# Optimization experiments

Hardware: AMD Instinct MI355X
Metric: run time of the kernel (lower is better)

The kernel has to match this reference:

```python
import jax, jax.numpy as jnp
import numpy as np

B, N, D_MODEL, H = 8, 1024, 768, 12
HD = D_MODEL // H  # head dim = 64
SCALE = D_MODEL ** (-0.5)  # NOTE: original scales by input_dim**-0.5, not head_dim**-0.5


def setup_inputs() -> dict:
    key = jax.random.key(0)
    k1, k2 = jax.random.split(key)
    x = jax.random.normal(k1, (B, N, D_MODEL), dtype=jnp.float32)
    # torch Linear weight is [out,in]; we store transposed [in,out] for x @ W
    w_qkv = jax.random.normal(k2, (D_MODEL, 3 * D_MODEL), dtype=jnp.float32) * (D_MODEL ** -0.5)
    b_qkv = jnp.zeros((3 * D_MODEL,), dtype=jnp.float32)
    return {"x": x, "w_qkv": w_qkv, "b_qkv": b_qkv}


def reference(x, w_qkv, b_qkv):
    # QKV projection: [B, N, 3*D]
    y = jnp.einsum("bnd,de->bne", x, w_qkv) + b_qkv
    # Faithful to einops 'b n (h d qkv) -> qkv b h n d': qkv is fastest-varying
    y = y.reshape(B, N, H, HD, 3)
    q = jnp.transpose(y[..., 0], (0, 2, 1, 3))  # [B, H, N, HD]
    k = jnp.transpose(y[..., 1], (0, 2, 1, 3))
    v = jnp.transpose(y[..., 2], (0, 2, 1, 3))
    energy = jnp.einsum("bhqd,bhkd->bhqk", q, k)
    attn = jax.nn.softmax(energy * SCALE, axis=-1)  # dropout is identity at eval
    out = jnp.einsum("bhqk,bhkd->bhqd", attn, v)
    # 'b h n d -> b n (h d)'
    return jnp.transpose(out, (0, 2, 1, 3)).reshape(B, N, D_MODEL)
```

## Files before the change

kernel.cpp:

```cpp
#include <hip/hip_runtime.h>
#include <hip/hip_bf16.h>
#include <stdint.h>

#define NB 8
#define NS 1024
#define DM 768
#define NH 12
#define DH 64
#define NE 2304
#define MTOT (NB*NS)

typedef unsigned short u16;
typedef __attribute__((ext_vector_type(8))) __bf16 bf16x8;
typedef __attribute__((ext_vector_type(4))) float floatx4;

#define WS_XB  0ull
#define WS_WT  12582912ull
#define WS_QB  16121856ull
#define WS_KB  28704768ull
#define WS_VT  41287680ull

__device__ __forceinline__ u16 f2bf(float f) {
  union { float f; uint32_t u; } v; v.f = f;
  uint32_t r = (v.u + 0x7fffu + ((v.u >> 16) & 1u)) >> 16;
  return (u16)r;
}

__device__ __forceinline__ void gload16(const void* g, void* l) {
  __builtin_amdgcn_global_load_lds(
      (const __attribute__((address_space(1))) void*)g,
      (__attribute__((address_space(3))) void*)l, 16, 0, 0);
}

__global__ void conv_x_kernel(const float4* __restrict__ x, u16* __restrict__ xb, int n4) {
  int i = blockIdx.x * blockDim.x + threadIdx.x;
  int stride = gridDim.x * blockDim.x;
  for (; i < n4; i += stride) {
    float4 v = x[i];
    ushort4 r;
    r.x = f2bf(v.x); r.y = f2bf(v.y); r.z = f2bf(v.z); r.w = f2bf(v.w);
    ((ushort4*)xb)[i] = r;
  }
}

__global__ void transpose_w_kernel(const float* __restrict__ w, u16* __restrict__ wt) {
  __shared__ float tile[32][33];
  const int e0 = blockIdx.x * 32, k0 = blockIdx.y * 32;
  const int tx = threadIdx.x, ty = threadIdx.y;
#pragma unroll
  for (int i = 0; i < 4; i++)
    tile[ty + i*8][tx] = w[(size_t)(k0 + ty + i*8) * NE + e0 + tx];
  __syncthreads();
#pragma unroll
  for (int i = 0; i < 4; i++)
    wt[(size_t)(e0 + ty + i*8) * DM + k0 + tx] = f2bf(tile[tx][ty + i*8]);
}

__global__ __launch_bounds__(256) void qkv_gemm_kernel(
    const u16* __restrict__ xb, const u16* __restrict__ wt,
    const float* __restrict__ bias,
    u16* __restrict__ qb, u16* __restrict__ kb, u16* __restrict__ vtb) {
  __shared__ __align__(16) u16 a_lds[128 * 32];
  __shared__ __align__(16) u16 b_lds[128 * 32];
  const int t  = threadIdx.x;
  const int w  = t >> 6, l = t & 63;
  const int wr = w >> 1, wc = w & 1;
  const int lq = l & 15, lg = l >> 4;
  const int m0 = (int)(blockIdx.x % 64) * 128;
  const int n0 = (int)(blockIdx.x / 64) * 128;

  floatx4 z = {0.f, 0.f, 0.f, 0.f};
  floatx4 acc[4][4];
#pragma unroll
  for (int i = 0; i < 4; i++)
#pragma unroll
    for (int j = 0; j < 4; j++) acc[i][j] = z;

  const int srow = t >> 2;
  const int scb  = (t & 3) ^ ((t >> 3) & 3);
  const u16* ga = xb + (size_t)m0 * DM + scb * 8;
  const u16* gb = wt + (size_t)n0 * DM + scb * 8;
  const int rswz = (lq >> 1) & 3;

  for (int k0 = 0; k0 < DM; k0 += 32) {
#pragma unroll
    for (int i = 0; i < 2; i++) {
      gload16(ga + (size_t)(i*64 + srow) * DM + k0, (char*)a_lds + i*4096 + w*1024);
      gload16(gb + (size_t)(i*64 + srow) * DM + k0, (char*)b_lds + i*4096 + w*1024);
    }
    __syncthreads();

    bf16x8 af[4], bfr[4];
#pragma unroll
    for (int i = 0; i < 4; i++)
      af[i] = *(const bf16x8*)((const char*)a_lds + (wr*64 + i*16 + lq)*64 + ((lg ^ rswz) * 16));
#pragma unroll
    for (int j = 0; j < 4; j++)
      bfr[j] = *(const bf16x8*)((const char*)b_lds + (wc*64 + j*16 + lq)*64 + ((lg ^ rswz) * 16));
#pragma unroll
    for (int i = 0; i < 4; i++)
#pragma unroll
      for (int j = 0; j < 4; j++)
        acc[i][j] = __builtin_amdgcn_mfma_f32_16x16x32_bf16(af[i], bfr[j], acc[i][j], 0, 0, 0);
    __syncthreads();
  }

#pragma unroll
  for (int j = 0; j < 4; j++) {
    const int gn = n0 + wc*64 + j*16 + lq;
    const float bv = bias[gn];
    const int qkv = gn % 3;
    const int h   = gn / 192;
    const int d   = (gn % 192) / 3;
#pragma unroll
    for (int i = 0; i < 4; i++) {
      const int gmb = m0 + wr*64 + i*16 + lg*4;
#pragma unroll
      for (int r = 0; r < 4; r++) {
        const int gm = gmb + r;
        const int bb = gm >> 10, nn = gm & 1023;
        const int bh = bb * NH + h;
        const u16 val = f2bf(acc[i][j][r] + bv);
        if (qkv == 0)      qb[((size_t)bh * NS + nn) * DH + d] = val;
        else if (qkv == 1) kb[((size_t)bh * NS + nn) * DH + d] = val;
        else               vtb[((size_t)bh * DH + d) * NS + nn] = val;
      }
    }
  }
}

__global__ __launch_bounds__(256) void attn_kernel(
    const u16* __restrict__ qb, const u16* __restrict__ kb,
    const u16* __restrict__ vtb, float* __restrict__ out) {
  __shared__ __align__(16) u16 k_lds[64 * 64];
  __shared__ __align__(16) u16 v_lds[64 * 64];
  __shared__ __align__(16) u16 p_lds[4][16 * 40];

  const int t = threadIdx.x, w = t >> 6, l = t & 63;
  const int bh = blockIdx.x >> 3, qblk = blockIdx.x & 7;
  const int bb = bh / NH, h = bh % NH;
  const int q0 = qblk * 128 + w * 32;
  const int lq = l & 15, lg = l >> 4;

  const float cscale = 0.03608439182435161f * 1.4426950408889634f;

  bf16x8 qf[2][2];
#pragma unroll
  for (int qt = 0; qt < 2; qt++) {
    const u16* qrow = qb + ((size_t)bh * NS + q0 + qt*16 + lq) * DH;
#pragma unroll
    for (int ds = 0; ds < 2; ds++)
      qf[qt][ds] = *(const bf16x8*)&qrow[lg*8 + ds*32];
  }

  float m2[2]   = {-1e30f, -1e30f};
  float lsum[2] = {0.f, 0.f};
  floatx4 z = {0.f, 0.f, 0.f, 0.f};
  floatx4 o[2][4];
#pragma unroll
  for (int qt = 0; qt < 2; qt++)
#pragma unroll
    for (int dt = 0; dt < 4; dt++) o[qt][dt] = z;

  const int srow = t >> 3;
  const int scb  = (t & 7) ^ ((t >> 3) & 7);

  for (int kt0 = 0; kt0 < 16; kt0++) {
    const int k0 = kt0 * 64;
    __syncthreads();
#pragma unroll
    for (int i = 0; i < 2; i++) {
      const int row = i*32 + srow;
      gload16(kb  + ((size_t)bh * NS + k0 + row) * DH + scb*8, (char*)k_lds + i*4096 + w*1024);
      gload16(vtb + ((size_t)bh * DH + row) * NS + k0 + scb*8, (char*)v_lds + i*4096 + w*1024);
    }
    __syncthreads();

#pragma unroll
    for (int half = 0; half < 2; half++) {
#pragma unroll
      for (int qt = 0; qt < 2; qt++) {
        floatx4 st[2];
#pragma unroll
        for (int kt = 0; kt < 2; kt++) {
          st[kt] = z;
          const int row = half*32 + kt*16 + lq;
#pragma unroll
          for (int ds = 0; ds < 2; ds++) {
            const int cb = (lg + ds*4) ^ (row & 7);
            bf16x8 kf = *(const bf16x8*)((const char*)k_lds + row*128 + cb*16);
            st[kt] = __builtin_amdgcn_mfma_f32_16x16x32_bf16(kf, qf[qt][ds], st[kt], 0, 0, 0);
          }
        }
        float s2[8], mt = -1e30f;
#pragma unroll
        for (int kt = 0; kt < 2; kt++)
#pragma unroll
          for (int r = 0; r < 4; r++) {
            float v = st[kt][r] * cscale;
            s2[kt*4 + r] = v;
            mt = fmaxf(mt, v);
          }
        mt = fmaxf(mt, __shfl_xor(mt, 16));
        mt = fmaxf(mt, __shfl_xor(mt, 32));
        const float mnew = fmaxf(m2[qt], mt);
        const float corr = exp2f(m2[qt] - mnew);
        m2[qt] = mnew;
        float ps = 0.f;
        u16 pb[8];
#pragma unroll
        for (int e = 0; e < 8; e++) {
          float p = exp2f(s2[e] - mnew);
          ps += p;
          pb[e] = f2bf(p);
        }
        ps += __shfl_xor(ps, 16);
        ps += __shfl_xor(ps, 32);
        lsum[qt] = lsum[qt] * corr + ps;

#pragma unroll
        for (int kt = 0; kt < 2; kt++) {
          ushort4 pk;
          pk.x = pb[kt*4+0]; pk.y = pb[kt*4+1]; pk.z = pb[kt*4+2]; pk.w = pb[kt*4+3];
          *(ushort4*)&p_lds[w][lq*40 + kt*16 + lg*4] = pk;
        }
        float cr[4];
#pragma unroll
        for (int r = 0; r < 4; r++) cr[r] = __shfl(corr, lg*4 + r);
#pragma unroll
        for (int dt = 0; dt < 4; dt++)
#pragma unroll
          for (int r = 0; r < 4; r++) o[qt][dt][r] *= cr[r];

        bf16x8 pa = *(const bf16x8*)&p_lds[w][lq*40 + lg*8];
#pragma unroll
        for (int dt = 0; dt < 4; dt++) {
          const int row = dt*16 + lq;
          const int cb = (half*4 + lg) ^ (row & 7);
          bf16x8 vf = *(const bf16x8*)((const char*)v_lds + row*128 + cb*16);
          o[qt][dt] = __builtin_amdgcn_mfma_f32_16x16x32_bf16(pa, vf, o[qt][dt], 0, 0, 0);
        }
      }
    }
  }

#pragma unroll
  for (int qt = 0; qt < 2; qt++) {
    const float inv = 1.0f / lsum[qt];
    float ir[4];
#pragma unroll
    for (int r = 0; r < 4; r++) ir[r] = __shfl(inv, lg*4 + r);
#pragma unroll
    for (int dt = 0; dt < 4; dt++)
#pragma unroll
      for (int r = 0; r < 4; r++) {
        const int n = q0 + qt*16 + lg*4 + r;
        out[((size_t)bb * NS + n) * DM + h*DH + dt*16 + lq] = o[qt][dt][r] * ir[r];
      }
  }
}

extern "C" void kernel_launch(void* const* d_in, const int* in_sizes, int n_in,
                              void* d_out, int out_size, void* d_ws, size_t ws_size,
                              hipStream_t stream) {
  const float* x     = (const float*)d_in[0];
  const float* w_qkv = (const float*)d_in[1];
  const float* b_qkv = (const float*)d_in[2];
  float* out = (float*)d_out;
  char* ws = (char*)d_ws;

  u16* xb  = (u16*)(ws + WS_XB);
  u16* wt  = (u16*)(ws + WS_WT);
  u16* qb  = (u16*)(ws + WS_QB);
  u16* kb  = (u16*)(ws + WS_KB);
  u16* vtb = (u16*)(ws + WS_VT);

  conv_x_kernel<<<1024, 256, 0, stream>>>((const float4*)x, xb, MTOT * DM / 4);
  transpose_w_kernel<<<dim3(NE/32, DM/32), dim3(32, 8), 0, stream>>>(w_qkv, wt);
  qkv_gemm_kernel<<<64 * (NE/128), 256, 0, stream>>>(xb, wt, b_qkv, qb, kb, vtb);
  attn_kernel<<<(NB*NH) * (NS/128), 256, 0, stream>>>(qb, kb, vtb, out);
}
```

Measured before the change: 146.8 us.

## Fold softmax scale into Q, keep P in registers, use lazy max rescaling

```diff
diff --git a/kernel.cpp b/kernel.cpp
--- a/kernel.cpp
+++ b/kernel.cpp
@@ -13,12 +13,15 @@
 typedef unsigned short u16;
 typedef __attribute__((ext_vector_type(8))) __bf16 bf16x8;
 typedef __attribute__((ext_vector_type(4))) float floatx4;
+typedef __attribute__((ext_vector_type(4))) uint32_t uint32x4;
 
 #define WS_XB  0ull
 #define WS_WT  12582912ull
 #define WS_QB  16121856ull
 #define WS_KB  28704768ull
 #define WS_VT  41287680ull
+
+#define QSC 0.05206490030275093f
 
 __device__ __forceinline__ u16 f2bf(float f) {
   union { float f; uint32_t u; } v; v.f = f;
@@ -120,7 +123,9 @@
         const int gm = gmb + r;
         const int bb = gm >> 10, nn = gm & 1023;
         const int bh = bb * NH + h;
-        const u16 val = f2bf(acc[i][j][r] + bv);
+        float ov = acc[i][j][r] + bv;
+        if (qkv == 0) ov *= QSC;
+        const u16 val = f2bf(ov);
         if (qkv == 0)      qb[((size_t)bh * NS + nn) * DH + d] = val;
         else if (qkv == 1) kb[((size_t)bh * NS + nn) * DH + d] = val;
         else               vtb[((size_t)bh * DH + d) * NS + nn] = val;
@@ -134,7 +139,6 @@
     const u16* __restrict__ vtb, float* __restrict__ out) {
   __shared__ __align__(16) u16 k_lds[64 * 64];
   __shared__ __align__(16) u16 v_lds[64 * 64];
-  __shared__ __align__(16) u16 p_lds[4][16 * 40];
 
   const int t = threadIdx.x, w = t >> 6, l = t & 63;
   const int bh = blockIdx.x >> 3, qblk = blockIdx.x & 7;
@@ -142,8 +146,6 @@
   const int q0 = qblk * 128 + w * 32;
   const int lq = l & 15, lg = l >> 4;
 
-  const float cscale = 0.03608439182435161f * 1.4426950408889634f;
-
   bf16x8 qf[2][2];
 #pragma unroll
   for (int qt = 0; qt < 2; qt++) {
@@ -153,8 +155,8 @@
       qf[qt][ds] = *(const bf16x8*)&qrow[lg*8 + ds*32];
   }
 
-  float m2[2]   = {-1e30f, -1e30f};
-  float lsum[2] = {0.f, 0.f};
+  float m2[2]    = {4.0f, 4.0f};
+  float lsumP[2] = {0.f, 0.f};
   floatx4 z = {0.f, 0.f, 0.f, 0.f};
   floatx4 o[2][4];
 #pragma unroll
@@ -163,7 +165,7 @@
     for (int dt = 0; dt < 4; dt++) o[qt][dt] = z;
 
   const int srow = t >> 3;
-  const int scb  = (t & 7) ^ ((t >> 3) & 7);
+  const int scb  = (t & 7) ^ (srow & 7);
 
   for (int kt0 = 0; kt0 < 16; kt0++) {
     const int k0 = kt0 * 64;
@@ -178,75 +180,83 @@
 
 #pragma unroll
     for (int half = 0; half < 2; half++) {
+      bf16x8 kf[2][2];
+#pragma unroll
+      for (int kt = 0; kt < 2; kt++) {
+        const int krow = half*32 + ((lq >> 2) << 3) + kt*4 + (lq & 3);
+#pragma unroll
+        for (int ds = 0; ds < 2; ds++)
+          kf[kt][ds] = *(const bf16x8*)((const char*)k_lds + krow*128 + ((ds*4 + lg) ^ (krow & 7))*16);
+      }
+      bf16x8 vf[4];
+#pragma unroll
+      for (int dt = 0; dt < 4; dt++) {
+        const int vrow = dt*16 + lq;
+        vf[dt] = *(const bf16x8*)((const char*)v_lds + vrow*128 + ((half*4 + lg) ^ (vrow & 7))*16);
+      }
+
 #pragma unroll
       for (int qt = 0; qt < 2; qt++) {
-        floatx4 st[2];
-#pragma unroll
-        for (int kt = 0; kt < 2; kt++) {
-          st[kt] = z;
-          const int row = half*32 + kt*16 + lq;
-#pragma unroll
-          for (int ds = 0; ds < 2; ds++) {
-            const int cb = (lg + ds*4) ^ (row & 7);
-            bf16x8 kf = *(const bf16x8*)((const char*)k_lds + row*128 + cb*16);
-            st[kt] = __builtin_amdgcn_mfma_f32_16x16x32_bf16(kf, qf[qt][ds], st[kt], 0, 0, 0);
-          }
+        floatx4 st0 = z, st1 = z;
+        st0 = __builtin_amdgcn_mfma_f32_16x16x32_bf16(kf[0][0], qf[qt][0], st0, 0, 0, 0);
+        st0 = __builtin_amdgcn_mfma_f32_16x16x32_bf16(kf[0][1], qf[qt][1], st0, 0, 0, 0);
+        st1 = __builtin_amdgcn_mfma_f32_16x16x32_bf16(kf[1][0], qf[qt][0], st1, 0, 0, 0);
+        st1 = __builtin_amdgcn_mfma_f32_16x16x32_bf16(kf[1][1], qf[qt][1], st1, 0, 0, 0);
+
+        float p[8];
+#pragma unroll
+        for (int r = 0; r < 4; r++) { p[r] = st0[r]; p[4 + r] = st1[r]; }
+        const float pmax = fmaxf(fmaxf(fmaxf(p[0], p[1]), fmaxf(p[2], p[3])),
+                                 fmaxf(fmaxf(p[4], p[5]), fmaxf(p[6], p[7])));
+
+        if (!__all(pmax - m2[qt] <= 8.0f)) {
+          float mt = pmax;
+          mt = fmaxf(mt, __shfl_xor(mt, 16));
+          mt = fmaxf(mt, __shfl_xor(mt, 32));
+          const float mnew = fmaxf(m2[qt], mt);
+          const float corr = exp2f(m2[qt] - mnew);
+          lsumP[qt] *= corr;
+          float cr[4];
+#pragma unroll
+          for (int r = 0; r < 4; r++) cr[r] = __shfl(corr, lg*4 + r);
+#pragma unroll
+          for (int dt = 0; dt < 4; dt++)
+#pragma unroll
+            for (int r = 0; r < 4; r++) o[qt][dt][r] *= cr[r];
+          m2[qt] = mnew;
         }
-        float s2[8], mt = -1e30f;
-#pragma unroll
-        for (int kt = 0; kt < 2; kt++)
-#pragma unroll
-          for (int r = 0; r < 4; r++) {
-            float v = st[kt][r] * cscale;
-            s2[kt*4 + r] = v;
-            mt = fmaxf(mt, v);
-          }
-        mt = fmaxf(mt, __shfl_xor(mt, 16));
-        mt = fmaxf(mt, __shfl_xor(mt, 32));
-        const float mnew = fmaxf(m2[qt], mt);
-        const float corr = exp2f(m2[qt] - mnew);
-        m2[qt] = mnew;
-        float ps = 0.f;
+
+        const float m = m2[qt];
+        float ls = 0.f;
         u16 pb[8];
 #pragma unroll
         for (int e = 0; e < 8; e++) {
-          float p = exp2f(s2[e] - mnew);
-          ps += p;
-          pb[e] = f2bf(p);
+          const float pe = exp2f(p[e] - m);
+          ls += pe;
+          pb[e] = f2bf(pe);
         }
-        ps += __shfl_xor(ps, 16);
-        ps += __shfl_xor(ps, 32);
-        lsum[qt] = lsum[qt] * corr + ps;
-
-#pragma unroll
-        for (int kt = 0; kt < 2; kt++) {
-          ushort4 pk;
-          pk.x = pb[kt*4+0]; pk.y = pb[kt*4+1]; pk.z = pb[kt*4+2]; pk.w = pb[kt*4+3];
-          *(ushort4*)&p_lds[w][lq*40 + kt*16 + lg*4] = pk;
-        }
-        float cr[4];
-#pragma unroll
-        for (int r = 0; r < 4; r++) cr[r] = __shfl(corr, lg*4 + r);
+        lsumP[qt] += ls;
+
+        uint32x4 pw;
+        pw.x = (uint32_t)pb[0] | ((uint32_t)pb[1] << 16);
+        pw.y = (uint32_t)pb[2] | ((uint32_t)pb[3] << 16);
+        pw.z = (uint32_t)pb[4] | ((uint32_t)pb[5] << 16);
+        pw.w = (uint32_t)pb[6] | ((uint32_t)pb[7] << 16);
+        const bf16x8 pa = __builtin_bit_cast(bf16x8, pw);
+
 #pragma unroll
         for (int dt = 0; dt < 4; dt++)
-#pragma unroll
-          for (int r = 0; r < 4; r++) o[qt][dt][r] *= cr[r];
-
-        bf16x8 pa = *(const bf16x8*)&p_lds[w][lq*40 + lg*8];
-#pragma unroll
-        for (int dt = 0; dt < 4; dt++) {
-          const int row = dt*16 + lq;
-          const int cb = (half*4 + lg) ^ (row & 7);
-          bf16x8 vf = *(const bf16x8*)((const char*)v_lds + row*128 + cb*16);
-          o[qt][dt] = __builtin_amdgcn_mfma_f32_16x16x32_bf16(pa, vf, o[qt][dt], 0, 0, 0);
-        }
+          o[qt][dt] = __builtin_amdgcn_mfma_f32_16x16x32_bf16(pa, vf[dt], o[qt][dt], 0, 0, 0);
       }
     }
   }
 
 #pragma unroll
   for (int qt = 0; qt < 2; qt++) {
-    const float inv = 1.0f / lsum[qt];
+    float ls = lsumP[qt];
+    ls += __shfl_xor(ls, 16);
+    ls += __shfl_xor(ls, 32);
+    const float inv = 1.0f / ls;
     float ir[4];
 #pragma unroll
     for (int r = 0; r < 4; r++) ir[r] = __shfl(inv, lg*4 + r);
```

Result: faster. 122.5 us (-16.6%).
